# Optimization experiments

Measured on AMD Instinct MI355X. Metric: run time of the kernel, lower is better.

## Reference

```python
import jax, jax.numpy as jnp
import numpy as np
from jax import lax

DIM = 128  # per-head dim used for scaling


def setup_inputs() -> dict:
    key = jax.random.key(0)
    ks = jax.random.split(key, 6)
    B, S, D = 16, 2048, DIM
    query = jax.random.normal(ks[0], (B, S, D), dtype=jnp.float32)
    k = jax.random.normal(ks[1], (B, S, D), dtype=jnp.float32)
    value = jax.random.normal(ks[2], (B, S, D), dtype=jnp.float32)
    mask = jax.random.randint(ks[3], (B, 1, S), 0, 2, dtype=jnp.int32)
    conv_w = jax.random.normal(ks[4], (B, 1, 3, 3), dtype=jnp.float32) * 0.1  # depthwise 3x3, OIHW
    conv_b = jax.random.normal(ks[5], (B,), dtype=jnp.float32) * 0.1
    return {"query": query, "key": k, "value": value, "mask": mask,
            "conv_w": conv_w, "conv_b": conv_b}


def reference(query, key, value, mask, conv_w, conv_b):
    B = query.shape[0]
    # score: (B, Sq, Sk)
    score = jnp.einsum('bqd,bkd->bqk', query, key) / jnp.float32(np.sqrt(DIM))
    # depthwise 3x3 conv over the score map; score treated as (C=B, H=Sq, W=Sk)
    conv = lax.conv_general_dilated(
        score[None],                      # (1, B, Sq, Sk)
        conv_w,                           # (B, 1, 3, 3)
        window_strides=(1, 1), padding='SAME',
        feature_group_count=B,
        dimension_numbers=('NCHW', 'OIHW', 'NCHW'))[0]
    conv = jax.nn.relu(conv + conv_b[:, None, None])
    conv_score = score + conv
    conv_score = jnp.where(mask == 0, jnp.float32(-1e9), conv_score)
    atten = jax.nn.softmax(conv_score, axis=-1)  # attn_drop=0.0 -> identity
    context = jnp.einsum('bqk,bkd->bqd', atten, value)
    return (context, atten)
```

## Files before the change

kernel.cpp:

```cpp
#include <hip/hip_runtime.h>
#include <stdint.h>

#define B_BATCH 16
#define SEQ     2048
#define DIMD    128
#define QT_OUT  28
#define SROWS   30
#define TILES_PB 74
#define SCALE   0.08838834764831845f
#define L2E     1.4426950408889634f

#define SC_STRIDE 4096
#define STG_OFF   (SROWS * SC_STRIDE)
#define LDS_TOTAL (STG_OFF + 2 * 16384)

typedef __attribute__((ext_vector_type(8))) short bf16x8;
typedef __attribute__((ext_vector_type(4))) float f32x4;

__device__ __forceinline__ unsigned short f2bf(float f) {
  union { float f; uint32_t u; } v; v.f = f;
  uint32_t u = v.u;
  return (unsigned short)((u + 0x7FFFu + ((u >> 16) & 1u)) >> 16);
}
__device__ __forceinline__ float bf2f(unsigned short h) {
  union { uint32_t u; float f; } v; v.u = ((uint32_t)h) << 16;
  return v.f;
}
__device__ __forceinline__ void gll16(const void* g, void* l) {
  __builtin_amdgcn_global_load_lds(
      (const __attribute__((address_space(1))) unsigned int*)g,
      (__attribute__((address_space(3))) unsigned int*)l, 16, 0, 0);
}

__global__ __launch_bounds__(256) void cvt_bf16(const float* __restrict__ in,
                                                unsigned short* __restrict__ out) {
  const size_t i = (size_t)blockIdx.x * 256 + threadIdx.x;
  const float4 a = *(const float4*)(in + i * 8);
  const float4 b = *(const float4*)(in + i * 8 + 4);
  uint4 o;
  o.x = (uint32_t)f2bf(a.x) | ((uint32_t)f2bf(a.y) << 16);
  o.y = (uint32_t)f2bf(a.z) | ((uint32_t)f2bf(a.w) << 16);
  o.z = (uint32_t)f2bf(b.x) | ((uint32_t)f2bf(b.y) << 16);
  o.w = (uint32_t)f2bf(b.z) | ((uint32_t)f2bf(b.w) << 16);
  *(uint4*)(out + i * 8) = o;
}

__global__ __launch_bounds__(256) void transpose_v(const float* __restrict__ V,
                                                   unsigned short* __restrict__ Vt) {
  __shared__ float tl[64][65];
  const int b  = blockIdx.x >> 6;
  const int kt = (blockIdx.x & 63) >> 1;
  const int dt = blockIdx.x & 1;
  const int k0 = kt * 64, d0 = dt * 64;
  const int tid = threadIdx.x;
  const int r = tid >> 4, c4 = (tid & 15) * 4;
  const float* Vb = V + (size_t)b * SEQ * DIMD;
#pragma unroll
  for (int ii = 0; ii < 4; ++ii) {
    const int row = ii * 16 + r;
    float4 v = *(const float4*)(Vb + (size_t)(k0 + row) * DIMD + d0 + c4);
    tl[row][c4 + 0] = v.x; tl[row][c4 + 1] = v.y;
    tl[row][c4 + 2] = v.z; tl[row][c4 + 3] = v.w;
  }
  __syncthreads();
  unsigned short* VtB = Vt + (size_t)b * DIMD * SEQ;
#pragma unroll
  for (int ii = 0; ii < 4; ++ii) {
    const int drow = ii * 16 + r;
    ushort4 o;
    o.x = f2bf(tl[c4 + 0][drow]); o.y = f2bf(tl[c4 + 1][drow]);
    o.z = f2bf(tl[c4 + 2][drow]); o.w = f2bf(tl[c4 + 3][drow]);
    *(ushort4*)(VtB + (size_t)(d0 + drow) * SEQ + k0 + c4) = o;
  }
}

__global__ __launch_bounds__(512) void fused_attn(
    const float* __restrict__ Q, const unsigned short* __restrict__ Kb,
    const unsigned short* __restrict__ Vt, const int* __restrict__ msk,
    const float* __restrict__ cw, const float* __restrict__ cbv,
    float* __restrict__ ctx, float* __restrict__ attn) {
  __shared__ __align__(16) char smem[LDS_TOTAL];
  char* buf0 = smem + STG_OFF;
  char* buf1 = buf0 + 16384;

  const int bid = blockIdx.x;
  const int b  = bid / TILES_PB;
  const int t  = bid - b * TILES_PB;
  const int g0 = t * QT_OUT;
  const int tid = threadIdx.x;
  const int w = tid >> 6, lane = tid & 63, l15 = lane & 15, hi = lane >> 4;

  float w9[9];
#pragma unroll
  for (int i = 0; i < 9; ++i) w9[i] = cw[b * 9 + i];
  const float bias = cbv[b];

  uint32_t mb = 0;
  {
    const int* mp = msk + b * SEQ;
#pragma unroll
    for (int jb = 0; jb < 8; ++jb) {
      int4 mv = *(const int4*)(mp + jb * 256 + lane * 4);
      mb |= (mv.x != 0 ? 1u : 0u) << (jb * 4 + 0);
      mb |= (mv.y != 0 ? 1u : 0u) << (jb * 4 + 1);
      mb |= (mv.z != 0 ? 1u : 0u) << (jb * 4 + 2);
      mb |= (mv.w != 0 ? 1u : 0u) << (jb * 4 + 3);
    }
  }

  bf16x8 aq[2][4];
#pragma unroll
  for (int qt = 0; qt < 2; ++qt) {
    int grow = g0 - 1 + qt * 16 + l15;
    grow = grow < 0 ? 0 : (grow > SEQ - 1 ? SEQ - 1 : grow);
    const float* qp = Q + ((size_t)(b * SEQ + grow)) * DIMD + hi * 8;
#pragma unroll
    for (int ks = 0; ks < 4; ++ks) {
      float4 x = *(const float4*)(qp + ks * 32);
      float4 y = *(const float4*)(qp + ks * 32 + 4);
      bf16x8 f;
      f[0] = (short)f2bf(x.x); f[1] = (short)f2bf(x.y);
      f[2] = (short)f2bf(x.z); f[3] = (short)f2bf(x.w);
      f[4] = (short)f2bf(y.x); f[5] = (short)f2bf(y.y);
      f[6] = (short)f2bf(y.z); f[7] = (short)f2bf(y.w);
      aq[qt][ks] = f;
    }
  }

  const unsigned short* KbB = Kb + (size_t)b * SEQ * DIMD;
  {
#pragma unroll
    for (int s = 0; s < 2; ++s) {
      int sl = w * 2 + s;
      int o = sl * 1024 + lane * 16;
      int krow = o >> 8;
      int cc = ((o >> 4) & 15) ^ (krow & 7);
      gll16(KbB + (size_t)krow * DIMD + cc * 8, buf0 + sl * 1024);
    }
  }
  __syncthreads();

  const int kw = w >> 1, qt1 = w & 1;
  for (int c = 0; c < 32; ++c) {
    if (c + 1 < 32) {
      char* nb = (c & 1) ? buf0 : buf1;
#pragma unroll
      for (int s = 0; s < 2; ++s) {
        int sl = w * 2 + s;
        int o = sl * 1024 + lane * 16;
        int krow = o >> 8;
        int cc = ((o >> 4) & 15) ^ (krow & 7);
        gll16(KbB + (size_t)((c + 1) * 64 + krow) * DIMD + cc * 8, nb + sl * 1024);
      }
    }
    const char* cbuf = (c & 1) ? buf1 : buf0;
    f32x4 acc = {0.f, 0.f, 0.f, 0.f};
    const int krl = kw * 16 + l15;
    const int ksw = (krl & 7) << 4;
#pragma unroll
    for (int ks = 0; ks < 4; ++ks) {
      bf16x8 bf = *(const bf16x8*)(cbuf + krl * 256 + ((ks * 64 + hi * 16) ^ ksw));
      acc = __builtin_amdgcn_mfma_f32_16x16x32_bf16(aq[qt1][ks], bf, acc, 0, 0, 0);
    }
    const int col2 = (c * 64 + kw * 16 + l15) * 2;
#pragma unroll
    for (int r = 0; r < 4; ++r) {
      int row = qt1 * 16 + hi * 4 + r;
      if (row < SROWS) {
        *(unsigned short*)(smem + row * SC_STRIDE + (col2 ^ ((row & 7) << 4))) =
            f2bf(acc[r] * SCALE);
      }
    }
    __syncthreads();
  }

  const int nrows = (SEQ - g0) < QT_OUT ? (SEQ - g0) : QT_OUT;
  float* attnB = attn + (size_t)b * SEQ * SEQ;

  for (int sp = 0; sp < 4; ++sp) {
    const int i = sp * 8 + w;
    const bool act = (i < nrows);
    float p[32];
    float inv = 0.f;
    if (act) {
      const int g = g0 + i;
      const bool vtop = (g > 0);
      const bool vbot = (g + 1 < SEQ);
#pragma unroll
      for (int jb = 0; jb < 8; ++jb) {
        const int colb = jb * 256 + lane * 4;
        float M[4][3], Lv[3], Rv[3];
#pragma unroll
        for (int r = 0; r < 3; ++r) {
          const int row = i + r;
          const bool v = (r == 1) || ((r == 0) ? vtop : vbot);
          if (v) {
            const int rs = row * SC_STRIDE, sw = (row & 7) << 4;
            ushort4 mm = *(const ushort4*)(smem + rs + ((colb * 2) ^ sw));
            M[0][r] = bf2f(mm.x); M[1][r] = bf2f(mm.y);
            M[2][r] = bf2f(mm.z); M[3][r] = bf2f(mm.w);
            Lv[r] = (colb > 0)
                        ? bf2f(*(const unsigned short*)(smem + rs + (((colb - 1) * 2) ^ sw)))
                        : 0.f;
            Rv[r] = (colb + 4 < SEQ)
                        ? bf2f(*(const unsigned short*)(smem + rs + (((colb + 4) * 2) ^ sw)))
                        : 0.f;
          } else {
            M[0][r] = 0.f; M[1][r] = 0.f; M[2][r] = 0.f; M[3][r] = 0.f;
            Lv[r] = 0.f; Rv[r] = 0.f;
          }
        }
#pragma unroll
        for (int c = 0; c < 4; ++c) {
          float cv = 0.f;
#pragma unroll
          for (int r = 0; r < 3; ++r) {
            const float lft = (c == 0) ? Lv[r] : M[c - 1][r];
            const float rgt = (c == 3) ? Rv[r] : M[c + 1][r];
            cv += w9[r * 3 + 0] * lft + w9[r * 3 + 1] * M[c][r] + w9[r * 3 + 2] * rgt;
          }
          const float val = M[c][1] + fmaxf(cv + bias, 0.f);
          p[jb * 4 + c] = ((mb >> (jb * 4 + c)) & 1u) ? val : -1e9f;
        }
      }
      float mx = p[0];
#pragma unroll
      for (int k = 1; k < 32; ++k) mx = fmaxf(mx, p[k]);
#pragma unroll
      for (int o = 1; o < 64; o <<= 1) mx = fmaxf(mx, __shfl_xor(mx, o, 64));
      float Z = 0.f;
#pragma unroll
      for (int k = 0; k < 32; ++k) { p[k] = exp2f((p[k] - mx) * L2E); Z += p[k]; }
#pragma unroll
      for (int o = 1; o < 64; o <<= 1) Z += __shfl_xor(Z, o, 64);
      inv = 1.0f / Z;
      float* arow = attnB + (size_t)g * SEQ;
#pragma unroll
      for (int jb = 0; jb < 8; ++jb) {
        float4 o4 = make_float4(p[jb * 4 + 0] * inv, p[jb * 4 + 1] * inv,
                                p[jb * 4 + 2] * inv, p[jb * 4 + 3] * inv);
        *(float4*)(arow + jb * 256 + lane * 4) = o4;
      }
    }
    __syncthreads();
    if (act) {
      const int rs = i * SC_STRIDE, sw = (i & 7) << 4;
#pragma unroll
      for (int jb = 0; jb < 8; ++jb) {
        ushort4 h;
        h.x = f2bf(p[jb * 4 + 0] * inv); h.y = f2bf(p[jb * 4 + 1] * inv);
        h.z = f2bf(p[jb * 4 + 2] * inv); h.w = f2bf(p[jb * 4 + 3] * inv);
        *(ushort4*)(smem + rs + ((jb * 512 + lane * 8) ^ sw)) = h;
      }
    }
    __syncthreads();
  }

  const unsigned short* VtB = Vt + (size_t)b * DIMD * SEQ;
  f32x4 acc0 = {0.f, 0.f, 0.f, 0.f}, acc1 = {0.f, 0.f, 0.f, 0.f};
  const int qbase = (w & 1) * 14;
  const int dp = w >> 1;
  {
#pragma unroll
    for (int s = 0; s < 2; ++s) {
      int sl = w * 2 + s;
      int o = sl * 1024 + lane * 16;
      int d = o >> 7;
      int cc = ((o >> 4) & 7) ^ (d & 7);
      gll16(VtB + (size_t)d * SEQ + cc * 8, buf0 + sl * 1024);
    }
  }
  __syncthreads();

  const int arw = qbase + l15;
  const int asw = (arw & 7) << 4;
  for (int c = 0; c < 32; ++c) {
    if (c + 1 < 32) {
      char* nb = (c & 1) ? buf0 : buf1;
#pragma unroll
      for (int s = 0; s < 2; ++s) {
        int sl = w * 2 + s;
        int o = sl * 1024 + lane * 16;
        int d = o >> 7;
        int cc = ((o >> 4) & 7) ^ (d & 7);
        gll16(VtB + (size_t)d * SEQ + (c + 1) * 64 + cc * 8, nb + sl * 1024);
      }
    }
    const char* cbuf = (c & 1) ? buf1 : buf0;
#pragma unroll
    for (int ks = 0; ks < 2; ++ks) {
      bf16x8 af = *(const bf16x8*)(smem + arw * SC_STRIDE +
                                   ((c * 128 + ks * 64 + hi * 16) ^ asw));
#pragma unroll
      for (int dd = 0; dd < 2; ++dd) {
        const int d = (dp * 2 + dd) * 16 + l15;
        bf16x8 bf = *(const bf16x8*)(cbuf + d * 128 +
                                     ((ks * 64 + hi * 16) ^ ((d & 7) << 4)));
        if (dd == 0) acc0 = __builtin_amdgcn_mfma_f32_16x16x32_bf16(af, bf, acc0, 0, 0, 0);
        else         acc1 = __builtin_amdgcn_mfma_f32_16x16x32_bf16(af, bf, acc1, 0, 0, 0);
      }
    }
    __syncthreads();
  }

#pragma unroll
  for (int dd = 0; dd < 2; ++dd) {
    const int col = (dp * 2 + dd) * 16 + l15;
    const f32x4 a = dd ? acc1 : acc0;
#pragma unroll
    for (int r = 0; r < 4; ++r) {
      const int row = hi * 4 + r;
      if (row <= 13) {
        const int g = g0 + qbase + row;
        if (g < SEQ) ctx[((size_t)(b * SEQ + g)) * DIMD + col] = a[r];
      }
    }
  }
}

extern "C" void kernel_launch(void* const* d_in, const int* in_sizes, int n_in,
                              void* d_out, int out_size, void* d_ws, size_t ws_size,
                              hipStream_t stream) {
  const float* Q  = (const float*)d_in[0];
  const float* K  = (const float*)d_in[1];
  const float* V  = (const float*)d_in[2];
  const int* msk  = (const int*)d_in[3];
  const float* cw = (const float*)d_in[4];
  const float* cb = (const float*)d_in[5];
  float* ctx  = (float*)d_out;
  float* attn = ctx + (size_t)B_BATCH * SEQ * DIMD;
  unsigned short* Kb = (unsigned short*)d_ws;
  unsigned short* Vt = Kb + (size_t)B_BATCH * SEQ * DIMD;

  cvt_bf16<<<2048, 256, 0, stream>>>(K, Kb);
  transpose_v<<<B_BATCH * 64, 256, 0, stream>>>(V, Vt);
  fused_attn<<<B_BATCH * TILES_PB, 512, 0, stream>>>(Q, Kb, Vt, msk, cw, cb, ctx, attn);
}
```

Baseline: 361.1 us.

## Halve query tile, drop LDS staging, load K/V directly from global

Shrinks the per-block query tile from 28 to 14 output rows (16 score rows), which doubles the block count. LDS use drops to 64KB so more blocks fit per CU, with launch bounds asking for 4. The double-buffered global_load_lds staging of K and Vt is removed: each wave reads its own K rows and Vt columns straight from global memory into registers, removing the per-chunk barriers. The conv/softmax stage now reads 8 contiguous columns per lane with shuffle-based neighbour exchange and uses the hardware exp2. The trade-off is that K and V are re-read from L2 twice as often, since the 3-row halo overhead is amortised over fewer output rows.

New measurement: 413.3 us. 1.14x slower.

```diff
diff --git a/kernel.cpp b/kernel.cpp
--- a/kernel.cpp
+++ b/kernel.cpp
@@ -4,15 +4,14 @@
 #define B_BATCH 16
 #define SEQ     2048
 #define DIMD    128
-#define QT_OUT  28
-#define SROWS   30
-#define TILES_PB 74
+#define QT_OUT  14
+#define SROWS   16
+#define TILES_PB 147
 #define SCALE   0.08838834764831845f
 #define L2E     1.4426950408889634f
 
 #define SC_STRIDE 4096
-#define STG_OFF   (SROWS * SC_STRIDE)
-#define LDS_TOTAL (STG_OFF + 2 * 16384)
+#define LDS_TOTAL (SROWS * SC_STRIDE)
 
 typedef __attribute__((ext_vector_type(8))) short bf16x8;
 typedef __attribute__((ext_vector_type(4))) float f32x4;
@@ -25,11 +24,6 @@
 __device__ __forceinline__ float bf2f(unsigned short h) {
   union { uint32_t u; float f; } v; v.u = ((uint32_t)h) << 16;
   return v.f;
-}
-__device__ __forceinline__ void gll16(const void* g, void* l) {
-  __builtin_amdgcn_global_load_lds(
-      (const __attribute__((address_space(1))) unsigned int*)g,
-      (__attribute__((address_space(3))) unsigned int*)l, 16, 0, 0);
 }
 
 __global__ __launch_bounds__(256) void cvt_bf16(const float* __restrict__ in,
@@ -74,14 +68,12 @@
   }
 }
 
-__global__ __launch_bounds__(512) void fused_attn(
+__global__ __launch_bounds__(512, 4) void fused_attn(
     const float* __restrict__ Q, const unsigned short* __restrict__ Kb,
     const unsigned short* __restrict__ Vt, const int* __restrict__ msk,
     const float* __restrict__ cw, const float* __restrict__ cbv,
     float* __restrict__ ctx, float* __restrict__ attn) {
   __shared__ __align__(16) char smem[LDS_TOTAL];
-  char* buf0 = smem + STG_OFF;
-  char* buf1 = buf0 + 16384;
 
   const int bid = blockIdx.x;
   const int b  = bid / TILES_PB;
@@ -99,19 +91,23 @@
   {
     const int* mp = msk + b * SEQ;
 #pragma unroll
-    for (int jb = 0; jb < 8; ++jb) {
-      int4 mv = *(const int4*)(mp + jb * 256 + lane * 4);
-      mb |= (mv.x != 0 ? 1u : 0u) << (jb * 4 + 0);
-      mb |= (mv.y != 0 ? 1u : 0u) << (jb * 4 + 1);
-      mb |= (mv.z != 0 ? 1u : 0u) << (jb * 4 + 2);
-      mb |= (mv.w != 0 ? 1u : 0u) << (jb * 4 + 3);
-    }
-  }
-
-  bf16x8 aq[2][4];
-#pragma unroll
-  for (int qt = 0; qt < 2; ++qt) {
-    int grow = g0 - 1 + qt * 16 + l15;
+    for (int jb = 0; jb < 4; ++jb) {
+      int4 a = *(const int4*)(mp + jb * 512 + lane * 8);
+      int4 bq = *(const int4*)(mp + jb * 512 + lane * 8 + 4);
+      mb |= (a.x  != 0 ? 1u : 0u) << (jb * 8 + 0);
+      mb |= (a.y  != 0 ? 1u : 0u) << (jb * 8 + 1);
+      mb |= (a.z  != 0 ? 1u : 0u) << (jb * 8 + 2);
+      mb |= (a.w  != 0 ? 1u : 0u) << (jb * 8 + 3);
+      mb |= (bq.x != 0 ? 1u : 0u) << (jb * 8 + 4);
+      mb |= (bq.y != 0 ? 1u : 0u) << (jb * 8 + 5);
+      mb |= (bq.z != 0 ? 1u : 0u) << (jb * 8 + 6);
+      mb |= (bq.w != 0 ? 1u : 0u) << (jb * 8 + 7);
+    }
+  }
+
+  bf16x8 aq[4];
+  {
+    int grow = g0 - 1 + l15;
     grow = grow < 0 ? 0 : (grow > SEQ - 1 ? SEQ - 1 : grow);
     const float* qp = Q + ((size_t)(b * SEQ + grow)) * DIMD + hi * 8;
 #pragma unroll
@@ -123,104 +119,86 @@
       f[2] = (short)f2bf(x.z); f[3] = (short)f2bf(x.w);
       f[4] = (short)f2bf(y.x); f[5] = (short)f2bf(y.y);
       f[6] = (short)f2bf(y.z); f[7] = (short)f2bf(y.w);
-      aq[qt][ks] = f;
-    }
-  }
-
-  const unsigned short* KbB = Kb + (size_t)b * SEQ * DIMD;
-  {
-#pragma unroll
-    for (int s = 0; s < 2; ++s) {
-      int sl = w * 2 + s;
-      int o = sl * 1024 + lane * 16;
-      int krow = o >> 8;
-      int cc = ((o >> 4) & 15) ^ (krow & 7);
-      gll16(KbB + (size_t)krow * DIMD + cc * 8, buf0 + sl * 1024);
+      aq[ks] = f;
+    }
+  }
+
+  {
+    const unsigned short* KbB = Kb + (size_t)b * SEQ * DIMD;
+    const int k0w = w * 256;
+#pragma unroll 2
+    for (int kc = 0; kc < 16; ++kc) {
+      const int k0 = k0w + kc * 16;
+      const unsigned short* kp = KbB + (size_t)(k0 + l15) * DIMD + hi * 8;
+      bf16x8 bk0 = *(const bf16x8*)(kp);
+      bf16x8 bk1 = *(const bf16x8*)(kp + 32);
+      bf16x8 bk2 = *(const bf16x8*)(kp + 64);
+      bf16x8 bk3 = *(const bf16x8*)(kp + 96);
+      f32x4 acc = {0.f, 0.f, 0.f, 0.f};
+      acc = __builtin_amdgcn_mfma_f32_16x16x32_bf16(aq[0], bk0, acc, 0, 0, 0);
+      acc = __builtin_amdgcn_mfma_f32_16x16x32_bf16(aq[1], bk1, acc, 0, 0, 0);
+      acc = __builtin_amdgcn_mfma_f32_16x16x32_bf16(aq[2], bk2, acc, 0, 0, 0);
+      acc = __builtin_amdgcn_mfma_f32_16x16x32_bf16(aq[3], bk3, acc, 0, 0, 0);
+      const int colb = (k0 + l15) * 2;
+#pragma unroll
+      for (int r = 0; r < 4; ++r) {
+        const int row = hi * 4 + r;
+        *(unsigned short*)(smem + row * SC_STRIDE + (colb ^ ((row & 7) << 4))) =
+            f2bf(acc[r] * SCALE);
+      }
     }
   }
   __syncthreads();
-
-  const int kw = w >> 1, qt1 = w & 1;
-  for (int c = 0; c < 32; ++c) {
-    if (c + 1 < 32) {
-      char* nb = (c & 1) ? buf0 : buf1;
-#pragma unroll
-      for (int s = 0; s < 2; ++s) {
-        int sl = w * 2 + s;
-        int o = sl * 1024 + lane * 16;
-        int krow = o >> 8;
-        int cc = ((o >> 4) & 15) ^ (krow & 7);
-        gll16(KbB + (size_t)((c + 1) * 64 + krow) * DIMD + cc * 8, nb + sl * 1024);
-      }
-    }
-    const char* cbuf = (c & 1) ? buf1 : buf0;
-    f32x4 acc = {0.f, 0.f, 0.f, 0.f};
-    const int krl = kw * 16 + l15;
-    const int ksw = (krl & 7) << 4;
-#pragma unroll
-    for (int ks = 0; ks < 4; ++ks) {
-      bf16x8 bf = *(const bf16x8*)(cbuf + krl * 256 + ((ks * 64 + hi * 16) ^ ksw));
-      acc = __builtin_amdgcn_mfma_f32_16x16x32_bf16(aq[qt1][ks], bf, acc, 0, 0, 0);
-    }
-    const int col2 = (c * 64 + kw * 16 + l15) * 2;
-#pragma unroll
-    for (int r = 0; r < 4; ++r) {
-      int row = qt1 * 16 + hi * 4 + r;
-      if (row < SROWS) {
-        *(unsigned short*)(smem + row * SC_STRIDE + (col2 ^ ((row & 7) << 4))) =
-            f2bf(acc[r] * SCALE);
-      }
-    }
-    __syncthreads();
-  }
 
   const int nrows = (SEQ - g0) < QT_OUT ? (SEQ - g0) : QT_OUT;
   float* attnB = attn + (size_t)b * SEQ * SEQ;
 
-  for (int sp = 0; sp < 4; ++sp) {
+  for (int sp = 0; sp < 2; ++sp) {
     const int i = sp * 8 + w;
     const bool act = (i < nrows);
     float p[32];
     float inv = 0.f;
     if (act) {
       const int g = g0 + i;
-      const bool vtop = (g > 0);
-      const bool vbot = (g + 1 < SEQ);
-#pragma unroll
-      for (int jb = 0; jb < 8; ++jb) {
-        const int colb = jb * 256 + lane * 4;
-        float M[4][3], Lv[3], Rv[3];
+      const bool vtop = (g > 0), vbot = (g + 1 < SEQ);
+#pragma unroll
+      for (int jb = 0; jb < 4; ++jb) {
+        float m[3][8], Lv[3], Rv[3];
 #pragma unroll
         for (int r = 0; r < 3; ++r) {
-          const int row = i + r;
           const bool v = (r == 1) || ((r == 0) ? vtop : vbot);
           if (v) {
+            const int row = i + r;
             const int rs = row * SC_STRIDE, sw = (row & 7) << 4;
-            ushort4 mm = *(const ushort4*)(smem + rs + ((colb * 2) ^ sw));
-            M[0][r] = bf2f(mm.x); M[1][r] = bf2f(mm.y);
-            M[2][r] = bf2f(mm.z); M[3][r] = bf2f(mm.w);
-            Lv[r] = (colb > 0)
-                        ? bf2f(*(const unsigned short*)(smem + rs + (((colb - 1) * 2) ^ sw)))
-                        : 0.f;
-            Rv[r] = (colb + 4 < SEQ)
-                        ? bf2f(*(const unsigned short*)(smem + rs + (((colb + 4) * 2) ^ sw)))
-                        : 0.f;
+            bf16x8 vv = *(const bf16x8*)(smem + rs + ((jb * 1024 + lane * 16) ^ sw));
+#pragma unroll
+            for (int c = 0; c < 8; ++c) m[r][c] = bf2f((unsigned short)vv[c]);
+            float le = 0.f, re = 0.f;
+            if (jb > 0)
+              le = bf2f(*(const unsigned short*)(smem + rs + (((jb * 512 - 1) * 2) ^ sw)));
+            if (jb < 3)
+              re = bf2f(*(const unsigned short*)(smem + rs + (((jb * 512 + 512) * 2) ^ sw)));
+            const float lsh = __shfl_up(m[r][7], 1);
+            const float rsh = __shfl_down(m[r][0], 1);
+            Lv[r] = (lane == 0)  ? le : lsh;
+            Rv[r] = (lane == 63) ? re : rsh;
           } else {
-            M[0][r] = 0.f; M[1][r] = 0.f; M[2][r] = 0.f; M[3][r] = 0.f;
+#pragma unroll
+            for (int c = 0; c < 8; ++c) m[r][c] = 0.f;
             Lv[r] = 0.f; Rv[r] = 0.f;
           }
         }
 #pragma unroll
-        for (int c = 0; c < 4; ++c) {
+        for (int c = 0; c < 8; ++c) {
           float cv = 0.f;
 #pragma unroll
           for (int r = 0; r < 3; ++r) {
-            const float lft = (c == 0) ? Lv[r] : M[c - 1][r];
-            const float rgt = (c == 3) ? Rv[r] : M[c + 1][r];
-            cv += w9[r * 3 + 0] * lft + w9[r * 3 + 1] * M[c][r] + w9[r * 3 + 2] * rgt;
+            const float lft = (c == 0) ? Lv[r] : m[r][c - 1];
+            const float rgt = (c == 7) ? Rv[r] : m[r][c + 1];
+            cv += w9[r * 3 + 0] * lft + w9[r * 3 + 1] * m[r][c] + w9[r * 3 + 2] * rgt;
           }
-          const float val = M[c][1] + fmaxf(cv + bias, 0.f);
-          p[jb * 4 + c] = ((mb >> (jb * 4 + c)) & 1u) ? val : -1e9f;
+          const float val = m[1][c] + fmaxf(cv + bias, 0.f);
+          p[jb * 8 + c] = ((mb >> (jb * 8 + c)) & 1u) ? val : -1e9f;
         }
       }
       float mx = p[0];
@@ -230,90 +208,61 @@
       for (int o = 1; o < 64; o <<= 1) mx = fmaxf(mx, __shfl_xor(mx, o, 64));
       float Z = 0.f;
 #pragma unroll
-      for (int k = 0; k < 32; ++k) { p[k] = exp2f((p[k] - mx) * L2E); Z += p[k]; }
+      for (int k = 0; k < 32; ++k) {
+        p[k] = __builtin_amdgcn_exp2f((p[k] - mx) * L2E);
+        Z += p[k];
+      }
 #pragma unroll
       for (int o = 1; o < 64; o <<= 1) Z += __shfl_xor(Z, o, 64);
       inv = 1.0f / Z;
       float* arow = attnB + (size_t)g * SEQ;
 #pragma unroll
-      for (int jb = 0; jb < 8; ++jb) {
-        float4 o4 = make_float4(p[jb * 4 + 0] * inv, p[jb * 4 + 1] * inv,
-                                p[jb * 4 + 2] * inv, p[jb * 4 + 3] * inv);
-        *(float4*)(arow + jb * 256 + lane * 4) = o4;
+      for (int jb = 0; jb < 4; ++jb) {
+        const int colb = jb * 512 + lane * 8;
+        *(float4*)(arow + colb) = make_float4(p[jb * 8 + 0] * inv, p[jb * 8 + 1] * inv,
+                                              p[jb * 8 + 2] * inv, p[jb * 8 + 3] * inv);
+        *(float4*)(arow + colb + 4) = make_float4(p[jb * 8 + 4] * inv, p[jb * 8 + 5] * inv,
+                                                  p[jb * 8 + 6] * inv, p[jb * 8 + 7] * inv);
       }
     }
     __syncthreads();
     if (act) {
       const int rs = i * SC_STRIDE, sw = (i & 7) << 4;
 #pragma unroll
-      for (int jb = 0; jb < 8; ++jb) {
-        ushort4 h;
-        h.x = f2bf(p[jb * 4 + 0] * inv); h.y = f2bf(p[jb * 4 + 1] * inv);
-        h.z = f2bf(p[jb * 4 + 2] * inv); h.w = f2bf(p[jb * 4 + 3] * inv);
-        *(ushort4*)(smem + rs + ((jb * 512 + lane * 8) ^ sw)) = h;
+      for (int jb = 0; jb < 4; ++jb) {
+        bf16x8 h;
+#pragma unroll
+        for (int c = 0; c < 8; ++c) h[c] = (short)f2bf(p[jb * 8 + c] * inv);
+        *(bf16x8*)(smem + rs + ((jb * 1024 + lane * 16) ^ sw)) = h;
       }
     }
     __syncthreads();
   }
 
-  const unsigned short* VtB = Vt + (size_t)b * DIMD * SEQ;
-  f32x4 acc0 = {0.f, 0.f, 0.f, 0.f}, acc1 = {0.f, 0.f, 0.f, 0.f};
-  const int qbase = (w & 1) * 14;
-  const int dp = w >> 1;
-  {
-#pragma unroll
-    for (int s = 0; s < 2; ++s) {
-      int sl = w * 2 + s;
-      int o = sl * 1024 + lane * 16;
-      int d = o >> 7;
-      int cc = ((o >> 4) & 7) ^ (d & 7);
-      gll16(VtB + (size_t)d * SEQ + cc * 8, buf0 + sl * 1024);
-    }
-  }
-  __syncthreads();
-
-  const int arw = qbase + l15;
-  const int asw = (arw & 7) << 4;
-  for (int c = 0; c < 32; ++c) {
-    if (c + 1 < 32) {
-      char* nb = (c & 1) ? buf0 : buf1;
-#pragma unroll
-      for (int s = 0; s < 2; ++s) {
-        int sl = w * 2 + s;
-        int o = sl * 1024 + lane * 16;
-        int d = o >> 7;
-        int cc = ((o >> 4) & 7) ^ (d & 7);
-        gll16(VtB + (size_t)d * SEQ + (c + 1) * 64 + cc * 8, nb + sl * 1024);
-      }
-    }
-    const char* cbuf = (c & 1) ? buf1 : buf0;
-#pragma unroll
-    for (int ks = 0; ks < 2; ++ks) {
-      bf16x8 af = *(const bf16x8*)(smem + arw * SC_STRIDE +
-                                   ((c * 128 + ks * 64 + hi * 16) ^ asw));
-#pragma unroll
-      for (int dd = 0; dd < 2; ++dd) {
-        const int d = (dp * 2 + dd) * 16 + l15;
-        bf16x8 bf = *(const bf16x8*)(cbuf + d * 128 +
-                                     ((ks * 64 + hi * 16) ^ ((d & 7) << 4)));
-        if (dd == 0) acc0 = __builtin_amdgcn_mfma_f32_16x16x32_bf16(af, bf, acc0, 0, 0, 0);
-        else         acc1 = __builtin_amdgcn_mfma_f32_16x16x32_bf16(af, bf, acc1, 0, 0, 0);
-      }
-    }
-    __syncthreads();
-  }
-
-#pragma unroll
-  for (int dd = 0; dd < 2; ++dd) {
-    const int col = (dp * 2 + dd) * 16 + l15;
-    const f32x4 a = dd ? acc1 : acc0;
+  {
+    const unsigned short* vp =
+        Vt + (size_t)b * DIMD * SEQ + (size_t)(16 * w + l15) * SEQ + hi * 8;
+    const int arow = l15;
+    const int abase = arow * SC_STRIDE;
+    const int asw = (arow & 7) << 4;
+    f32x4 acc0 = {0.f, 0.f, 0.f, 0.f}, acc1 = {0.f, 0.f, 0.f, 0.f};
+#pragma unroll 2
+    for (int kc = 0; kc < 32; ++kc) {
+      const int k0 = kc * 64;
+      bf16x8 a0 = *(const bf16x8*)(smem + abase + (((k0      ) * 2 + hi * 16) ^ asw));
+      bf16x8 b0 = *(const bf16x8*)(vp + k0);
+      acc0 = __builtin_amdgcn_mfma_f32_16x16x32_bf16(a0, b0, acc0, 0, 0, 0);
+      bf16x8 a1 = *(const bf16x8*)(smem + abase + (((k0 + 32) * 2 + hi * 16) ^ asw));
+      bf16x8 b1 = *(const bf16x8*)(vp + k0 + 32);
+      acc1 = __builtin_amdgcn_mfma_f32_16x16x32_bf16(a1, b1, acc1, 0, 0, 0);
+    }
+    const int col = 16 * w + l15;
 #pragma unroll
     for (int r = 0; r < 4; ++r) {
       const int row = hi * 4 + r;
-      if (row <= 13) {
-        const int g = g0 + qbase + row;
-        if (g < SEQ) ctx[((size_t)(b * SEQ + g)) * DIMD + col] = a[r];
-      }
+      const int g = g0 + row;
+      if (row < QT_OUT && g < SEQ)
+        ctx[((size_t)(b * SEQ + g)) * DIMD + col] = acc0[r] + acc1[r];
     }
   }
 }
```
